# Optimization experiments

Hardware: AMD Instinct MI355X
Metric: run time of the kernel (lower is better)

## Reference

```python
import jax, jax.numpy as jnp
import numpy as np

BITS = 4
BLOCK_SIZE = 64
EPS = 1e-8


def nf_table():
    # NormalFloat table: inverse normal CDF at midpoints, normalized to [-1, 1].
    n_levels = 2 ** BITS
    p = (jnp.arange(n_levels, dtype=jnp.float32) + 0.5) / n_levels
    q = jax.scipy.special.ndtri(p)
    q = q / jnp.max(jnp.abs(q))
    return q.astype(jnp.float16)  # original stores table in fp16


def setup_inputs() -> dict:
    key = jax.random.key(0)
    x = jax.random.normal(key, (2048, 8192, 1), dtype=jnp.float32)
    return {"x": x}


def reference(x):
    table = nf_table()                          # (16,) fp16
    orig_shape = x.shape                        # (R, C, 1)
    R, C = orig_shape[0], orig_shape[1]
    nb = C // BLOCK_SIZE
    xb = x.reshape(R, nb, BLOCK_SIZE)           # (R, nb, bs)

    # --- compress ---
    x_min = jnp.min(xb, axis=2, keepdims=True)  # (R, nb, 1)
    x_max = jnp.max(xb, axis=2, keepdims=True)
    scales = jnp.squeeze(x_max - x_min, -1)     # (R, nb)
    x_norm = 2.0 * (xb - x_min) / (x_max - x_min + EPS) - 1.0
    # distance to each of 16 codebook levels, argmin over last axis
    dist = jnp.abs(x_norm[..., None] - table.astype(x_norm.dtype))  # (R, nb, bs, 16)
    q_idx = jnp.argmin(dist, axis=-1)           # (R, nb, bs) int

    # double quantization of scales (8-bit over each row)
    s_min = jnp.min(scales, axis=-1, keepdims=True)   # (R, 1)
    s_max = jnp.max(scales, axis=-1, keepdims=True)
    scales_q = jnp.round((scales - s_min) / (s_max - s_min + EPS) * 255.0)  # (R, nb)

    # --- decompress ---
    scales_rec = s_min + scales_q / 255.0 * (s_max - s_min)   # (R, nb)
    scales_rec = scales_rec[..., None]                        # (R, nb, 1)
    w_block = table[q_idx].astype(jnp.float32)                # (R, nb, bs)
    w_block = (w_block + 1.0) / 2.0 * scales_rec + x_min
    return w_block.reshape(orig_shape)
```

## Files before the change

kernel.cpp:

```cpp
#include <hip/hip_runtime.h>
#include <hip/hip_fp16.h>

#define C_COLS 8192

__global__ __launch_bounds__(256) void nf4_fused_kernel(
        const float* __restrict__ x, float* __restrict__ out) {
#pragma clang fp contract(off)
    __shared__ double zf[16];
    __shared__ float  stbl[16];
    __shared__ float  smin[4], smax[4];

    const int row  = blockIdx.x;
    const int wave = threadIdx.x >> 6;
    const int lane = threadIdx.x & 63;
    const long base = (long)row * C_COLS + (long)wave * 2048;
    const float4* __restrict__ xin4 = reinterpret_cast<const float4*>(x + base);
    float4* __restrict__ out4       = reinterpret_cast<float4*>(out + base);

    float4 v[8];
#pragma unroll
    for (int k = 0; k < 8; ++k) v[k] = xin4[k * 64 + lane];

    if (threadIdx.x < 16) {
        const int i = threadIdx.x;
        double p  = (2.0 * i + 1.0) / 32.0;
        double pl = (p < 0.5) ? p : 1.0 - p;
        double t  = sqrt(-2.0 * log(pl));
        double z  = t - (2.30753 + 0.27061 * t) / (1.0 + t * (0.99229 + 0.04481 * t));
        if (p < 0.5) z = -z;
        for (int it = 0; it < 3; ++it) {
            double Phi = 0.5 * erfc(-z * 0.7071067811865476);
            double phi = 0.3989422804014326779 * exp(-0.5 * z * z);
            z -= (Phi - p) / phi;
        }
        zf[i] = z;
    }
    __syncthreads();
    if (threadIdx.x < 16) {
        float zi = (float)zf[threadIdx.x];
        float qmax = 0.0f;
        for (int j = 0; j < 16; ++j) qmax = fmaxf(qmax, fabsf((float)zf[j]));
        float qn = zi / qmax;
        stbl[threadIdx.x] = __half2float(__float2half(qn));
    }

    float bmin[8], bmax[8], srec[8];
    float tmin = 3.4e38f, tmax = -3.4e38f;
#pragma unroll
    for (int k = 0; k < 8; ++k) {
        float m = fminf(fminf(v[k].x, v[k].y), fminf(v[k].z, v[k].w));
        float M = fmaxf(fmaxf(v[k].x, v[k].y), fmaxf(v[k].z, v[k].w));
#pragma unroll
        for (int off = 1; off < 16; off <<= 1) {
            m = fminf(m, __shfl_xor(m, off));
            M = fmaxf(M, __shfl_xor(M, off));
        }
        bmin[k] = m;
        bmax[k] = M;
        float sc = M - m;
        tmin = fminf(tmin, sc);
        tmax = fmaxf(tmax, sc);
    }
    tmin = fminf(tmin, __shfl_xor(tmin, 16));
    tmin = fminf(tmin, __shfl_xor(tmin, 32));
    tmax = fmaxf(tmax, __shfl_xor(tmax, 16));
    tmax = fmaxf(tmax, __shfl_xor(tmax, 32));

    if (lane == 0) { smin[wave] = tmin; smax[wave] = tmax; }
    __syncthreads();

    float tbl[16];
#pragma unroll
    for (int i = 0; i < 16; ++i) tbl[i] = stbl[i];

    const float s_min  = fminf(fminf(smin[0], smin[1]), fminf(smin[2], smin[3]));
    const float s_max  = fmaxf(fmaxf(smax[0], smax[1]), fmaxf(smax[2], smax[3]));
    const float srange = s_max - s_min;
    const float sden   = srange + 1e-8f;
    const float sqr    = 1.0f / sden;

#pragma unroll
    for (int k = 0; k < 8; ++k) {
        float sc = bmax[k] - bmin[k];
        float sq = rintf(((sc - s_min) * sqr) * 255.0f);
        srec[k]  = s_min + sq / 255.0f * srange;
    }

#pragma unroll
    for (int k = 0; k < 8; ++k) {
        const float bm  = bmin[k];
        const float den = (bmax[k] - bm) + 1e-8f;
        const float s2r = 2.0f / den;
        const float sr  = srec[k];
        float xv[4] = { v[k].x, v[k].y, v[k].z, v[k].w };
        float wv[4];
#pragma unroll
        for (int c = 0; c < 4; ++c) {
            float p  = (xv[c] - bm) * s2r;
            float xn = p - 1.0f;
            float best = fabsf(xn - tbl[0]);
            float tsel = tbl[0];
#pragma unroll
            for (int i = 1; i < 16; ++i) {
                float d = fabsf(xn - tbl[i]);
                if (d < best) { best = d; tsel = tbl[i]; }
            }
            wv[c] = (tsel + 1.0f) * 0.5f * sr + bm;
        }
        float4 r; r.x = wv[0]; r.y = wv[1]; r.z = wv[2]; r.w = wv[3];
        out4[k * 64 + lane] = r;
    }
}

extern "C" void kernel_launch(void* const* d_in, const int* in_sizes, int n_in,
                              void* d_out, int out_size, void* d_ws, size_t ws_size,
                              hipStream_t stream) {
    const float* x = (const float*)d_in[0];
    float* out     = (float*)d_out;
    const int rows = in_sizes[0] / C_COLS;
    nf4_fused_kernel<<<rows, 256, 0, stream>>>(x, out);
}
```

Baseline: 126.8 us.

## Replace 16-way codebook argmin with CDF-based index guess and neighbor check

```diff
diff --git a/kernel.cpp b/kernel.cpp
--- a/kernel.cpp
+++ b/kernel.cpp
@@ -1,14 +1,18 @@
 #include <hip/hip_runtime.h>
-#include <hip/hip_fp16.h>
+#include <cmath>
 
 #define C_COLS 8192
 
-__global__ __launch_bounds__(256) void nf4_fused_kernel(
-        const float* __restrict__ x, float* __restrict__ out) {
+struct NfArgs {
+    float tbl[16];
+    float kexp;
+};
+
+__global__ __launch_bounds__(256) void nf4_main_kernel(
+        const float* __restrict__ x, float* __restrict__ out, NfArgs args) {
 #pragma clang fp contract(off)
-    __shared__ double zf[16];
-    __shared__ float  stbl[16];
-    __shared__ float  smin[4], smax[4];
+    __shared__ float stbl[16];
+    __shared__ float smin[4], smax[4];
 
     const int row  = blockIdx.x;
     const int wave = threadIdx.x >> 6;
@@ -21,28 +25,7 @@
 #pragma unroll
     for (int k = 0; k < 8; ++k) v[k] = xin4[k * 64 + lane];
 
-    if (threadIdx.x < 16) {
-        const int i = threadIdx.x;
-        double p  = (2.0 * i + 1.0) / 32.0;
-        double pl = (p < 0.5) ? p : 1.0 - p;
-        double t  = sqrt(-2.0 * log(pl));
-        double z  = t - (2.30753 + 0.27061 * t) / (1.0 + t * (0.99229 + 0.04481 * t));
-        if (p < 0.5) z = -z;
-        for (int it = 0; it < 3; ++it) {
-            double Phi = 0.5 * erfc(-z * 0.7071067811865476);
-            double phi = 0.3989422804014326779 * exp(-0.5 * z * z);
-            z -= (Phi - p) / phi;
-        }
-        zf[i] = z;
-    }
-    __syncthreads();
-    if (threadIdx.x < 16) {
-        float zi = (float)zf[threadIdx.x];
-        float qmax = 0.0f;
-        for (int j = 0; j < 16; ++j) qmax = fmaxf(qmax, fabsf((float)zf[j]));
-        float qn = zi / qmax;
-        stbl[threadIdx.x] = __half2float(__float2half(qn));
-    }
+    if (threadIdx.x < 16) stbl[threadIdx.x] = args.tbl[threadIdx.x];
 
     float bmin[8], bmax[8], srec[8];
     float tmin = 3.4e38f, tmax = -3.4e38f;
@@ -69,10 +52,6 @@
     if (lane == 0) { smin[wave] = tmin; smax[wave] = tmax; }
     __syncthreads();
 
-    float tbl[16];
-#pragma unroll
-    for (int i = 0; i < 16; ++i) tbl[i] = stbl[i];
-
     const float s_min  = fminf(fminf(smin[0], smin[1]), fminf(smin[2], smin[3]));
     const float s_max  = fmaxf(fmaxf(smax[0], smax[1]), fmaxf(smax[2], smax[3]));
     const float srange = s_max - s_min;
@@ -86,6 +65,7 @@
         srec[k]  = s_min + sq / 255.0f * srange;
     }
 
+    const float kexp = args.kexp;
 #pragma unroll
     for (int k = 0; k < 8; ++k) {
         const float bm  = bmin[k];
@@ -98,18 +78,51 @@
         for (int c = 0; c < 4; ++c) {
             float p  = (xv[c] - bm) * s2r;
             float xn = p - 1.0f;
-            float best = fabsf(xn - tbl[0]);
-            float tsel = tbl[0];
-#pragma unroll
-            for (int i = 1; i < 16; ++i) {
-                float d = fabsf(xn - tbl[i]);
-                if (d < best) { best = d; tsel = tbl[i]; }
-            }
+            float eb = __builtin_amdgcn_exp2f(xn * kexp);
+            float f  = 16.0f * __builtin_amdgcn_rcpf(1.0f + eb);
+            int ci = (int)f;
+            ci = min(max(ci, 1), 14);
+            float tm1 = stbl[ci - 1];
+            float tc  = stbl[ci];
+            float tp1 = stbl[ci + 1];
+            float a0 = fabsf(xn - tm1);
+            float a1 = fabsf(xn - tc);
+            float a2 = fabsf(xn - tp1);
+            float t01  = (a1 < a0) ? tc : tm1;
+            float amin = fminf(a1, a0);
+            float tsel = (a2 < amin) ? tp1 : t01;
             wv[c] = (tsel + 1.0f) * 0.5f * sr + bm;
         }
         float4 r; r.x = wv[0]; r.y = wv[1]; r.z = wv[2]; r.w = wv[3];
         out4[k * 64 + lane] = r;
     }
+}
+
+static void compute_nf_args(NfArgs* a) {
+    double z[16];
+    for (int i = 0; i < 16; ++i) {
+        double p  = (2.0 * i + 1.0) / 32.0;
+        double pl = (p < 0.5) ? p : 1.0 - p;
+        double t  = std::sqrt(-2.0 * std::log(pl));
+        double zz = t - (2.30753 + 0.27061 * t) / (1.0 + t * (0.99229 + 0.04481 * t));
+        if (p < 0.5) zz = -zz;
+        for (int it = 0; it < 3; ++it) {
+            double Phi = 0.5 * std::erfc(-zz * 0.7071067811865476);
+            double phi = 0.3989422804014326779 * std::exp(-0.5 * zz * zz);
+            zz -= (Phi - p) / phi;
+        }
+        z[i] = zz;
+    }
+    float zf[16], qmax = 0.0f;
+    for (int i = 0; i < 16; ++i) { zf[i] = (float)z[i]; qmax = std::fmax(qmax, std::fabs(zf[i])); }
+    for (int i = 0; i < 16; ++i) {
+        float qn = zf[i] / qmax;
+        double av = std::fabs((double)qn);
+        int e; std::frexp(av, &e);
+        double ulp = std::ldexp(1.0, e - 11);
+        a->tbl[i] = (float)std::copysign(std::rint(av / ulp) * ulp, (double)qn);
+    }
+    a->kexp = (float)(-1.702 * 1.4426950408889634 * (double)qmax);
 }
 
 extern "C" void kernel_launch(void* const* d_in, const int* in_sizes, int n_in,
@@ -118,5 +131,9 @@
     const float* x = (const float*)d_in[0];
     float* out     = (float*)d_out;
     const int rows = in_sizes[0] / C_COLS;
-    nf4_fused_kernel<<<rows, 256, 0, stream>>>(x, out);
+
+    NfArgs args;
+    compute_nf_args(&args);
+
+    nf4_main_kernel<<<rows, 256, 0, stream>>>(x, out, args);
 }
```

New measurement: 112.4 us. -11.3%, faster.
